# Optimization experiments

Measured on AMD Instinct MI355X. Metric: run time of the kernel, lower is better.

Reference implementation:

```python
import jax, jax.numpy as jnp
import numpy as np

USER_NUM = 100000
ITEM_NUM = 200000
N_NODES = USER_NUM + ITEM_NUM
N_EDGES = 1250000
EMB = 64
N_LAYERS = 3


def setup_inputs() -> dict:
    key = jax.random.key(0)
    k1, k2, k3, k4, k5 = jax.random.split(key, 5)
    # xavier-like scale for embeddings
    scale = float(np.sqrt(6.0 / (N_NODES + EMB)))
    user_emb = jax.random.uniform(k1, (USER_NUM, EMB), jnp.float32, -scale, scale)
    item_emb = jax.random.uniform(k2, (ITEM_NUM, EMB), jnp.float32, -scale, scale)
    # COO sparse normalized adjacency over the full (user+item) node set
    adj_rows = jax.random.randint(k3, (N_EDGES,), 0, N_NODES, jnp.int32)
    adj_cols = jax.random.randint(k4, (N_EDGES,), 0, N_NODES, jnp.int32)
    adj_vals = jax.random.uniform(k5, (N_EDGES,), jnp.float32) * 0.1  # small normalized weights
    return {"user_emb": user_emb, "item_emb": item_emb, "adj_vals": adj_vals,
            "adj_rows": adj_rows, "adj_cols": adj_cols}


def _spmm(vals, rows, cols, x):
    # sparse [N,N] @ dense [N,d] via gather + segment_sum
    return jax.ops.segment_sum(vals[:, None] * x[cols], rows, num_segments=N_NODES)


def reference(user_emb, item_emb, adj_vals, adj_rows, adj_cols):
    ego = jnp.concatenate([user_emb, item_emb], axis=0)  # [N, d]
    acc = ego  # running sum over layers (fused alternative to stack+mean)
    for _ in range(N_LAYERS):
        ego = _spmm(adj_vals, adj_rows, adj_cols, ego)
        acc = acc + ego
    all_emb = acc / jnp.asarray(N_LAYERS + 1, dtype=acc.dtype)
    return all_emb[:USER_NUM], all_emb[USER_NUM:]
```

## Files before the change

kernel.cpp:

```cpp
#include <hip/hip_runtime.h>

#define USER_NUM 100000
#define ITEM_NUM 200000
#define N_NODES  300000
#define N_EDGES  1250000
#define EMB      64

constexpr int TOTAL_F4 = N_NODES * EMB / 4;
constexpr int USER_F4  = USER_NUM * EMB / 4;
constexpr int SCAN_CHUNK = 1024;
constexpr int NBLK = (N_NODES + SCAN_CHUNK - 1) / SCAN_CHUNK;

__global__ void lgcn_init_kernel(const float4* __restrict__ u, const float4* __restrict__ it,
                                 float4* __restrict__ out, float4* __restrict__ ego) {
    for (int i = blockIdx.x * blockDim.x + threadIdx.x; i < TOTAL_F4;
         i += gridDim.x * blockDim.x) {
        float4 v = (i < USER_F4) ? u[i] : it[i - USER_F4];
        out[i] = v;
        ego[i] = v;
    }
}


__global__ void hist_kernel(const int* __restrict__ rows, int* __restrict__ deg) {
    for (int e = blockIdx.x * blockDim.x + threadIdx.x; e < N_EDGES;
         e += gridDim.x * blockDim.x)
        atomicAdd(&deg[rows[e]], 1);
}

__global__ void scanA_kernel(int* __restrict__ deg, int* __restrict__ bsum) {
    __shared__ int s[256];
    int tid = threadIdx.x;
    int base = blockIdx.x * SCAN_CHUNK + tid * 4;
    int v[4];
#pragma unroll
    for (int k = 0; k < 4; ++k) v[k] = (base + k < N_NODES) ? deg[base + k] : 0;
    int tsum = v[0] + v[1] + v[2] + v[3];
    int val = tsum;
    s[tid] = val;
    __syncthreads();
    for (int off = 1; off < 256; off <<= 1) {
        int t = (tid >= off) ? s[tid - off] : 0;
        __syncthreads();
        val += t;
        s[tid] = val;
        __syncthreads();
    }
    if (tid == 255) bsum[blockIdx.x] = val;
    int run = val - tsum;
#pragma unroll
    for (int k = 0; k < 4; ++k) {
        if (base + k < N_NODES) deg[base + k] = run;
        run += v[k];
    }
}

__global__ void scanB_kernel(int* __restrict__ bsum) {
    __shared__ int s[512];
    int tid = threadIdx.x;
    int v = (tid < NBLK) ? bsum[tid] : 0;
    int val = v;
    s[tid] = val;
    __syncthreads();
    for (int off = 1; off < 512; off <<= 1) {
        int t = (tid >= off) ? s[tid - off] : 0;
        __syncthreads();
        val += t;
        s[tid] = val;
        __syncthreads();
    }
    if (tid < NBLK) bsum[tid] = val - v;
}

__global__ void scanC_kernel(const int* __restrict__ pre, const int* __restrict__ boff,
                             int* __restrict__ rowptr, int* __restrict__ wr) {
    int i = blockIdx.x * blockDim.x + threadIdx.x;
    if (i < N_NODES) {
        int p = pre[i] + boff[i / SCAN_CHUNK];
        rowptr[i] = p;
        wr[i] = p;
    }
    if (i == 0) rowptr[N_NODES] = N_EDGES;
}

__global__ void scatter_kernel(const int* __restrict__ rows, const int* __restrict__ cols,
                               const float* __restrict__ vals, int* __restrict__ wr,
                               int* __restrict__ pcols, float* __restrict__ pvals) {
    for (int e = blockIdx.x * blockDim.x + threadIdx.x; e < N_EDGES;
         e += gridDim.x * blockDim.x) {
        int r = rows[e];
        int p = atomicAdd(&wr[r], 1);
        pcols[p] = cols[e];
        pvals[p] = vals[e];
    }
}

template <int MODE>
__global__ void spmm_csr_kernel(const float4* __restrict__ x, const int* __restrict__ rowptr,
                                const int* __restrict__ pcols, const float* __restrict__ pvals,
                                float4* __restrict__ nxt, float4* __restrict__ out) {
    int gid = blockIdx.x * blockDim.x + threadIdx.x;
    int row = gid >> 4;
    if (row >= N_NODES) return;
    int t = gid & 15;
    int beg = rowptr[row];
    int end = rowptr[row + 1];
    float4 acc = {0.f, 0.f, 0.f, 0.f};
    for (int i = beg; i < end; ++i) {
        int c = pcols[i];
        float v = pvals[i];
        float4 xv = x[c * 16 + t];
        acc.x += v * xv.x;
        acc.y += v * xv.y;
        acc.z += v * xv.z;
        acc.w += v * xv.w;
    }
    int oi = row * 16 + t;
    float4 o = out[oi];
    if (MODE == 0) {
        nxt[oi] = acc;
        o.x += acc.x; o.y += acc.y; o.z += acc.z; o.w += acc.w;
    } else {
        o.x = (o.x + acc.x) * 0.25f;
        o.y = (o.y + acc.y) * 0.25f;
        o.z = (o.z + acc.z) * 0.25f;
        o.w = (o.w + acc.w) * 0.25f;
    }
    out[oi] = o;
}


__global__ void lgcn_spmm_atomic_kernel(const float* __restrict__ x, const float* __restrict__ vals,
                                        const int* __restrict__ rows, const int* __restrict__ cols,
                                        float* __restrict__ y) {
    int gid = blockIdx.x * blockDim.x + threadIdx.x;
    int e = gid >> 4;
    if (e >= N_EDGES) return;
    int t = gid & 15;
    int r = rows[e];
    int c = cols[e];
    float v = vals[e];
    float4 xv = *reinterpret_cast<const float4*>(x + (size_t)c * EMB + t * 4);
    float* yp = y + (size_t)r * EMB + t * 4;
    unsafeAtomicAdd(yp + 0, v * xv.x);
    unsafeAtomicAdd(yp + 1, v * xv.y);
    unsafeAtomicAdd(yp + 2, v * xv.z);
    unsafeAtomicAdd(yp + 3, v * xv.w);
}

__global__ void lgcn_accum_kernel(float4* __restrict__ out, const float4* __restrict__ nxt) {
    for (int i = blockIdx.x * blockDim.x + threadIdx.x; i < TOTAL_F4;
         i += gridDim.x * blockDim.x) {
        float4 o = out[i], n = nxt[i];
        o.x += n.x; o.y += n.y; o.z += n.z; o.w += n.w;
        out[i] = o;
    }
}

__global__ void lgcn_accum_scale_kernel(float4* __restrict__ out, const float4* __restrict__ nxt) {
    for (int i = blockIdx.x * blockDim.x + threadIdx.x; i < TOTAL_F4;
         i += gridDim.x * blockDim.x) {
        float4 o = out[i], n = nxt[i];
        o.x = (o.x + n.x) * 0.25f;
        o.y = (o.y + n.y) * 0.25f;
        o.z = (o.z + n.z) * 0.25f;
        o.w = (o.w + n.w) * 0.25f;
        out[i] = o;
    }
}

extern "C" void kernel_launch(void* const* d_in, const int* in_sizes, int n_in,
                              void* d_out, int out_size, void* d_ws, size_t ws_size,
                              hipStream_t stream) {
    const float* u    = (const float*)d_in[0];
    const float* it   = (const float*)d_in[1];
    const float* vals = (const float*)d_in[2];
    const int*   rows = (const int*)d_in[3];
    const int*   cols = (const int*)d_in[4];
    float* out = (float*)d_out;

    const size_t nelem = (size_t)N_NODES * EMB;
    const size_t nb    = nelem * sizeof(float);

    auto align256 = [](size_t x) { return (x + 255) & ~(size_t)255; };

    size_t off = 0;
    float* egoA = (float*)((char*)d_ws + off); off += align256(nb);
    float* egoB = (float*)((char*)d_ws + off); off += align256(nb);
    size_t csr_base = off;
    int*   deg    = (int*)((char*)d_ws + off); off += align256((size_t)N_NODES * 4);
    int*   bsum   = (int*)((char*)d_ws + off); off += align256(512 * 4);
    int*   rowptr = (int*)((char*)d_ws + off); off += align256((size_t)(N_NODES + 1) * 4);
    int*   wr     = (int*)((char*)d_ws + off); off += align256((size_t)N_NODES * 4);
    int*   pcols  = (int*)((char*)d_ws + off); off += align256((size_t)N_EDGES * 4);
    float* pvals  = (float*)((char*)d_ws + off); off += align256((size_t)N_EDGES * 4);
    bool have_csr = (ws_size >= off);
    (void)csr_base;

    if (ws_size < 2 * nb) return;

    lgcn_init_kernel<<<2048, 256, 0, stream>>>((const float4*)u, (const float4*)it,
                                               (float4*)out, (float4*)egoA);

    if (have_csr) {
        hipMemsetAsync(deg, 0, (size_t)N_NODES * 4, stream);
        hist_kernel<<<1024, 256, 0, stream>>>(rows, deg);
        scanA_kernel<<<NBLK, 256, 0, stream>>>(deg, bsum);
        scanB_kernel<<<1, 512, 0, stream>>>(bsum);
        scanC_kernel<<<(N_NODES + 255) / 256, 256, 0, stream>>>(deg, bsum, rowptr, wr);
        scatter_kernel<<<1024, 256, 0, stream>>>(rows, cols, vals, wr, pcols, pvals);

        const int spmm_blocks = (N_NODES * 16 + 255) / 256;
        spmm_csr_kernel<0><<<spmm_blocks, 256, 0, stream>>>(
            (const float4*)egoA, rowptr, pcols, pvals, (float4*)egoB, (float4*)out);
        spmm_csr_kernel<0><<<spmm_blocks, 256, 0, stream>>>(
            (const float4*)egoB, rowptr, pcols, pvals, (float4*)egoA, (float4*)out);
        spmm_csr_kernel<1><<<spmm_blocks, 256, 0, stream>>>(
            (const float4*)egoA, rowptr, pcols, pvals, nullptr, (float4*)out);
    } else {
        const int spmm_threads = N_EDGES * 16;
        const int spmm_blocks  = (spmm_threads + 255) / 256;
        float* cur = egoA;
        float* nxt = egoB;
        for (int l = 0; l < 3; ++l) {
            hipMemsetAsync(nxt, 0, nb, stream);
            lgcn_spmm_atomic_kernel<<<spmm_blocks, 256, 0, stream>>>(cur, vals, rows, cols, nxt);
            if (l < 2)
                lgcn_accum_kernel<<<2048, 256, 0, stream>>>((float4*)out, (const float4*)nxt);
            else
                lgcn_accum_scale_kernel<<<2048, 256, 0, stream>>>((float4*)out, (const float4*)nxt);
            float* tmp = cur; cur = nxt; nxt = tmp;
        }
    }
}
```

Measured before the change: 559.6 us.

## Fuse init and layer accumulation into SpMM kernels, pack CSR edges as int2

Drops the separate init copy kernel: the first SpMM reads user and item embeddings directly, and the last SpMM computes the layer mean from ego, layer 1, layer 2 and its own accumulator. This removes repeated read-modify-write of the output buffer across layers. Column index and value are packed into one int2 array so each edge needs a single load. The inner loop is unrolled by two with independent accumulators, and outputs use nontemporal stores. The atomic fallback path is removed, so the function now requires enough workspace for the CSR.

After: 478.0 us. -14.6%, faster.

```diff
diff --git a/kernel.cpp b/kernel.cpp
--- a/kernel.cpp
+++ b/kernel.cpp
@@ -6,19 +6,15 @@
 #define N_EDGES  1250000
 #define EMB      64
 
-constexpr int TOTAL_F4 = N_NODES * EMB / 4;
 constexpr int USER_F4  = USER_NUM * EMB / 4;
 constexpr int SCAN_CHUNK = 1024;
 constexpr int NBLK = (N_NODES + SCAN_CHUNK - 1) / SCAN_CHUNK;
 
-__global__ void lgcn_init_kernel(const float4* __restrict__ u, const float4* __restrict__ it,
-                                 float4* __restrict__ out, float4* __restrict__ ego) {
-    for (int i = blockIdx.x * blockDim.x + threadIdx.x; i < TOTAL_F4;
-         i += gridDim.x * blockDim.x) {
-        float4 v = (i < USER_F4) ? u[i] : it[i - USER_F4];
-        out[i] = v;
-        ego[i] = v;
-    }
+typedef float f32x4 __attribute__((ext_vector_type(4)));
+
+__device__ __forceinline__ void nt_store_f4(const float4& v, float4* p) {
+    f32x4 nv = {v.x, v.y, v.z, v.w};
+    __builtin_nontemporal_store(nv, reinterpret_cast<f32x4*>(p));
 }
 
 
@@ -85,88 +81,112 @@
 
 __global__ void scatter_kernel(const int* __restrict__ rows, const int* __restrict__ cols,
                                const float* __restrict__ vals, int* __restrict__ wr,
-                               int* __restrict__ pcols, float* __restrict__ pvals) {
+                               int2* __restrict__ pedge) {
     for (int e = blockIdx.x * blockDim.x + threadIdx.x; e < N_EDGES;
          e += gridDim.x * blockDim.x) {
         int r = rows[e];
         int p = atomicAdd(&wr[r], 1);
-        pcols[p] = cols[e];
-        pvals[p] = vals[e];
-    }
-}
-
-template <int MODE>
-__global__ void spmm_csr_kernel(const float4* __restrict__ x, const int* __restrict__ rowptr,
-                                const int* __restrict__ pcols, const float* __restrict__ pvals,
-                                float4* __restrict__ nxt, float4* __restrict__ out) {
+        int2 pk;
+        pk.x = cols[e];
+        pk.y = __float_as_int(vals[e]);
+        pedge[p] = pk;
+    }
+}
+
+
+__global__ void spmm_first_kernel(const float4* __restrict__ u, const float4* __restrict__ it,
+                                  const int* __restrict__ rowptr, const int2* __restrict__ pedge,
+                                  float4* __restrict__ y) {
     int gid = blockIdx.x * blockDim.x + threadIdx.x;
     int row = gid >> 4;
     if (row >= N_NODES) return;
     int t = gid & 15;
-    int beg = rowptr[row];
-    int end = rowptr[row + 1];
-    float4 acc = {0.f, 0.f, 0.f, 0.f};
-    for (int i = beg; i < end; ++i) {
-        int c = pcols[i];
-        float v = pvals[i];
-        float4 xv = x[c * 16 + t];
-        acc.x += v * xv.x;
-        acc.y += v * xv.y;
-        acc.z += v * xv.z;
-        acc.w += v * xv.w;
+    int beg = rowptr[row], end = rowptr[row + 1];
+    float4 a0 = {0.f, 0.f, 0.f, 0.f}, a1 = {0.f, 0.f, 0.f, 0.f};
+    int i = beg;
+    for (; i + 1 < end; i += 2) {
+        int2 e0 = pedge[i], e1 = pedge[i + 1];
+        const float4* p0 = (e0.x < USER_NUM) ? (u + e0.x * 16 + t) : (it + (e0.x - USER_NUM) * 16 + t);
+        const float4* p1 = (e1.x < USER_NUM) ? (u + e1.x * 16 + t) : (it + (e1.x - USER_NUM) * 16 + t);
+        float4 x0 = *p0, x1 = *p1;
+        float v0 = __int_as_float(e0.y), v1 = __int_as_float(e1.y);
+        a0.x += v0 * x0.x; a0.y += v0 * x0.y; a0.z += v0 * x0.z; a0.w += v0 * x0.w;
+        a1.x += v1 * x1.x; a1.y += v1 * x1.y; a1.z += v1 * x1.z; a1.w += v1 * x1.w;
+    }
+    if (i < end) {
+        int2 e0 = pedge[i];
+        const float4* p0 = (e0.x < USER_NUM) ? (u + e0.x * 16 + t) : (it + (e0.x - USER_NUM) * 16 + t);
+        float4 x0 = *p0;
+        float v0 = __int_as_float(e0.y);
+        a0.x += v0 * x0.x; a0.y += v0 * x0.y; a0.z += v0 * x0.z; a0.w += v0 * x0.w;
+    }
+    float4 acc = {a0.x + a1.x, a0.y + a1.y, a0.z + a1.z, a0.w + a1.w};
+    nt_store_f4(acc, &y[row * 16 + t]);
+}
+
+__global__ void spmm_mid_kernel(const float4* __restrict__ x, const int* __restrict__ rowptr,
+                                const int2* __restrict__ pedge, float4* __restrict__ y) {
+    int gid = blockIdx.x * blockDim.x + threadIdx.x;
+    int row = gid >> 4;
+    if (row >= N_NODES) return;
+    int t = gid & 15;
+    int beg = rowptr[row], end = rowptr[row + 1];
+    float4 a0 = {0.f, 0.f, 0.f, 0.f}, a1 = {0.f, 0.f, 0.f, 0.f};
+    int i = beg;
+    for (; i + 1 < end; i += 2) {
+        int2 e0 = pedge[i], e1 = pedge[i + 1];
+        float4 x0 = x[e0.x * 16 + t];
+        float4 x1 = x[e1.x * 16 + t];
+        float v0 = __int_as_float(e0.y), v1 = __int_as_float(e1.y);
+        a0.x += v0 * x0.x; a0.y += v0 * x0.y; a0.z += v0 * x0.z; a0.w += v0 * x0.w;
+        a1.x += v1 * x1.x; a1.y += v1 * x1.y; a1.z += v1 * x1.z; a1.w += v1 * x1.w;
+    }
+    if (i < end) {
+        int2 e0 = pedge[i];
+        float4 x0 = x[e0.x * 16 + t];
+        float v0 = __int_as_float(e0.y);
+        a0.x += v0 * x0.x; a0.y += v0 * x0.y; a0.z += v0 * x0.z; a0.w += v0 * x0.w;
+    }
+    float4 acc = {a0.x + a1.x, a0.y + a1.y, a0.z + a1.z, a0.w + a1.w};
+    nt_store_f4(acc, &y[row * 16 + t]);
+}
+
+__global__ void spmm_last_kernel(const float4* __restrict__ x,
+                                 const float4* __restrict__ e1,
+                                 const float4* __restrict__ u, const float4* __restrict__ it,
+                                 const int* __restrict__ rowptr, const int2* __restrict__ pedge,
+                                 float4* __restrict__ out) {
+    int gid = blockIdx.x * blockDim.x + threadIdx.x;
+    int row = gid >> 4;
+    if (row >= N_NODES) return;
+    int t = gid & 15;
+    int beg = rowptr[row], end = rowptr[row + 1];
+    float4 a0 = {0.f, 0.f, 0.f, 0.f}, a1 = {0.f, 0.f, 0.f, 0.f};
+    int i = beg;
+    for (; i + 1 < end; i += 2) {
+        int2 e0 = pedge[i], ee1 = pedge[i + 1];
+        float4 x0 = x[e0.x * 16 + t];
+        float4 x1 = x[ee1.x * 16 + t];
+        float v0 = __int_as_float(e0.y), v1 = __int_as_float(ee1.y);
+        a0.x += v0 * x0.x; a0.y += v0 * x0.y; a0.z += v0 * x0.z; a0.w += v0 * x0.w;
+        a1.x += v1 * x1.x; a1.y += v1 * x1.y; a1.z += v1 * x1.z; a1.w += v1 * x1.w;
+    }
+    if (i < end) {
+        int2 e0 = pedge[i];
+        float4 x0 = x[e0.x * 16 + t];
+        float v0 = __int_as_float(e0.y);
+        a0.x += v0 * x0.x; a0.y += v0 * x0.y; a0.z += v0 * x0.z; a0.w += v0 * x0.w;
     }
     int oi = row * 16 + t;
-    float4 o = out[oi];
-    if (MODE == 0) {
-        nxt[oi] = acc;
-        o.x += acc.x; o.y += acc.y; o.z += acc.z; o.w += acc.w;
-    } else {
-        o.x = (o.x + acc.x) * 0.25f;
-        o.y = (o.y + acc.y) * 0.25f;
-        o.z = (o.z + acc.z) * 0.25f;
-        o.w = (o.w + acc.w) * 0.25f;
-    }
-    out[oi] = o;
-}
-
-
-__global__ void lgcn_spmm_atomic_kernel(const float* __restrict__ x, const float* __restrict__ vals,
-                                        const int* __restrict__ rows, const int* __restrict__ cols,
-                                        float* __restrict__ y) {
-    int gid = blockIdx.x * blockDim.x + threadIdx.x;
-    int e = gid >> 4;
-    if (e >= N_EDGES) return;
-    int t = gid & 15;
-    int r = rows[e];
-    int c = cols[e];
-    float v = vals[e];
-    float4 xv = *reinterpret_cast<const float4*>(x + (size_t)c * EMB + t * 4);
-    float* yp = y + (size_t)r * EMB + t * 4;
-    unsafeAtomicAdd(yp + 0, v * xv.x);
-    unsafeAtomicAdd(yp + 1, v * xv.y);
-    unsafeAtomicAdd(yp + 2, v * xv.z);
-    unsafeAtomicAdd(yp + 3, v * xv.w);
-}
-
-__global__ void lgcn_accum_kernel(float4* __restrict__ out, const float4* __restrict__ nxt) {
-    for (int i = blockIdx.x * blockDim.x + threadIdx.x; i < TOTAL_F4;
-         i += gridDim.x * blockDim.x) {
-        float4 o = out[i], n = nxt[i];
-        o.x += n.x; o.y += n.y; o.z += n.z; o.w += n.w;
-        out[i] = o;
-    }
-}
-
-__global__ void lgcn_accum_scale_kernel(float4* __restrict__ out, const float4* __restrict__ nxt) {
-    for (int i = blockIdx.x * blockDim.x + threadIdx.x; i < TOTAL_F4;
-         i += gridDim.x * blockDim.x) {
-        float4 o = out[i], n = nxt[i];
-        o.x = (o.x + n.x) * 0.25f;
-        o.y = (o.y + n.y) * 0.25f;
-        o.z = (o.z + n.z) * 0.25f;
-        o.w = (o.w + n.w) * 0.25f;
-        out[i] = o;
-    }
+    float4 ego = (oi < USER_F4) ? u[oi] : it[oi - USER_F4];
+    float4 p1 = e1[oi];
+    float4 p2 = x[oi];
+    float4 o;
+    o.x = (ego.x + p1.x + p2.x + a0.x + a1.x) * 0.25f;
+    o.y = (ego.y + p1.y + p2.y + a0.y + a1.y) * 0.25f;
+    o.z = (ego.z + p1.z + p2.z + a0.z + a1.z) * 0.25f;
+    o.w = (ego.w + p1.w + p2.w + a0.w + a1.w) * 0.25f;
+    nt_store_f4(o, &out[oi]);
 }
 
 extern "C" void kernel_launch(void* const* d_in, const int* in_sizes, int n_in,
@@ -185,51 +205,30 @@
     auto align256 = [](size_t x) { return (x + 255) & ~(size_t)255; };
 
     size_t off = 0;
-    float* egoA = (float*)((char*)d_ws + off); off += align256(nb);
-    float* egoB = (float*)((char*)d_ws + off); off += align256(nb);
-    size_t csr_base = off;
+    float* bufA = (float*)((char*)d_ws + off); off += align256(nb);
+    float* bufB = (float*)((char*)d_ws + off); off += align256(nb);
     int*   deg    = (int*)((char*)d_ws + off); off += align256((size_t)N_NODES * 4);
     int*   bsum   = (int*)((char*)d_ws + off); off += align256(512 * 4);
     int*   rowptr = (int*)((char*)d_ws + off); off += align256((size_t)(N_NODES + 1) * 4);
     int*   wr     = (int*)((char*)d_ws + off); off += align256((size_t)N_NODES * 4);
-    int*   pcols  = (int*)((char*)d_ws + off); off += align256((size_t)N_EDGES * 4);
-    float* pvals  = (float*)((char*)d_ws + off); off += align256((size_t)N_EDGES * 4);
-    bool have_csr = (ws_size >= off);
-    (void)csr_base;
-
-    if (ws_size < 2 * nb) return;
-
-    lgcn_init_kernel<<<2048, 256, 0, stream>>>((const float4*)u, (const float4*)it,
-                                               (float4*)out, (float4*)egoA);
-
-    if (have_csr) {
-        hipMemsetAsync(deg, 0, (size_t)N_NODES * 4, stream);
-        hist_kernel<<<1024, 256, 0, stream>>>(rows, deg);
-        scanA_kernel<<<NBLK, 256, 0, stream>>>(deg, bsum);
-        scanB_kernel<<<1, 512, 0, stream>>>(bsum);
-        scanC_kernel<<<(N_NODES + 255) / 256, 256, 0, stream>>>(deg, bsum, rowptr, wr);
-        scatter_kernel<<<1024, 256, 0, stream>>>(rows, cols, vals, wr, pcols, pvals);
-
-        const int spmm_blocks = (N_NODES * 16 + 255) / 256;
-        spmm_csr_kernel<0><<<spmm_blocks, 256, 0, stream>>>(
-            (const float4*)egoA, rowptr, pcols, pvals, (float4*)egoB, (float4*)out);
-        spmm_csr_kernel<0><<<spmm_blocks, 256, 0, stream>>>(
-            (const float4*)egoB, rowptr, pcols, pvals, (float4*)egoA, (float4*)out);
-        spmm_csr_kernel<1><<<spmm_blocks, 256, 0, stream>>>(
-            (const float4*)egoA, rowptr, pcols, pvals, nullptr, (float4*)out);
-    } else {
-        const int spmm_threads = N_EDGES * 16;
-        const int spmm_blocks  = (spmm_threads + 255) / 256;
-        float* cur = egoA;
-        float* nxt = egoB;
-        for (int l = 0; l < 3; ++l) {
-            hipMemsetAsync(nxt, 0, nb, stream);
-            lgcn_spmm_atomic_kernel<<<spmm_blocks, 256, 0, stream>>>(cur, vals, rows, cols, nxt);
-            if (l < 2)
-                lgcn_accum_kernel<<<2048, 256, 0, stream>>>((float4*)out, (const float4*)nxt);
-            else
-                lgcn_accum_scale_kernel<<<2048, 256, 0, stream>>>((float4*)out, (const float4*)nxt);
-            float* tmp = cur; cur = nxt; nxt = tmp;
-        }
-    }
-}
+    int2*  pedge  = (int2*)((char*)d_ws + off); off += align256((size_t)N_EDGES * 8);
+
+    if (ws_size < off) return;
+
+    (void)hipMemsetAsync(deg, 0, (size_t)N_NODES * 4, stream);
+    hist_kernel<<<1024, 256, 0, stream>>>(rows, deg);
+    scanA_kernel<<<NBLK, 256, 0, stream>>>(deg, bsum);
+    scanB_kernel<<<1, 512, 0, stream>>>(bsum);
+    scanC_kernel<<<(N_NODES + 255) / 256, 256, 0, stream>>>(deg, bsum, rowptr, wr);
+    scatter_kernel<<<1024, 256, 0, stream>>>(rows, cols, vals, wr, pedge);
+
+    const int spmm_blocks = (N_NODES * 16 + 255) / 256;
+
+    spmm_first_kernel<<<spmm_blocks, 256, 0, stream>>>(
+        (const float4*)u, (const float4*)it, rowptr, pedge, (float4*)bufB);
+    spmm_mid_kernel<<<spmm_blocks, 256, 0, stream>>>(
+        (const float4*)bufB, rowptr, pedge, (float4*)bufA);
+    spmm_last_kernel<<<spmm_blocks, 256, 0, stream>>>(
+        (const float4*)bufA, (const float4*)bufB,
+        (const float4*)u, (const float4*)it, rowptr, pedge, (float4*)out);
+}
```
